# Performance work log

Measured on AMD Instinct MI355X. Metric: run time of the kernel, lower is better.

## Reference

```python
import jax, jax.numpy as jnp
import numpy as np

DEPTH_REF = jnp.array([28.01, 16.32], dtype=jnp.float32)
DIM_REF = jnp.array([[3.88, 1.63, 1.53], [0.84, 1.76, 0.66], [1.78, 1.52, 1.78]], dtype=jnp.float32)
TOPK = 50
DET_THRESHOLD = 0.25
PI = 3.14159265358979


def nms_hm(heat, kernel=3):
    # 3x3 max-pool NMS: keep peaks, zero everything else
    pad = (kernel - 1) // 2
    hmax = jax.lax.reduce_window(heat, -jnp.inf, jax.lax.max,
                                 (1, 1, kernel, kernel), (1, 1, 1, 1),
                                 [(0, 0), (0, 0), (pad, pad), (pad, pad)])
    return jnp.where(hmax == heat, heat, 0.0)


def select_topk(heat, K):
    B, C, H, W = heat.shape
    scores_all, inds_all = jax.lax.top_k(heat.reshape(B, C, H * W), K)  # [B,C,K]
    ys_all = (inds_all // W).astype(jnp.float32)
    xs_all = (inds_all % W).astype(jnp.float32)
    scores, inds = jax.lax.top_k(scores_all.reshape(B, C * K), K)       # [B,K] over classes
    clses = (inds // K).astype(jnp.float32)
    topk_inds = jnp.take_along_axis(inds_all.reshape(B, C * K), inds, axis=1)
    ys = jnp.take_along_axis(ys_all.reshape(B, C * K), inds, axis=1)
    xs = jnp.take_along_axis(xs_all.reshape(B, C * K), inds, axis=1)
    return scores, topk_inds, clses, ys, xs


def select_point_of_interest(index, feature_maps):
    B, Cf, H, W = feature_maps.shape
    fm = feature_maps.transpose(0, 2, 3, 1).reshape(B, H * W, Cf)
    return jnp.take_along_axis(fm, index[:, :, None], axis=1)  # [B,K,Cf]


def encode_box3d(rotys, dims, locs):
    # dims = (l, h, w); corner signs reproduce SMOKE's gather pattern
    N = rotys.shape[0]
    c, s = jnp.cos(rotys), jnp.sin(rotys)
    z, o = jnp.zeros_like(c), jnp.ones_like(c)
    ry = jnp.stack([c, z, s, z, o, z, -s, z, c], axis=1).reshape(N, 3, 3)
    sx = jnp.array([-0.5, 0.5, 0.5, 0.5, 0.5, -0.5, -0.5, -0.5], dtype=dims.dtype)
    sy = jnp.array([-1., -1., 0., 0., -1., -1., 0., 0.], dtype=dims.dtype)
    sz = jnp.array([-0.5, -0.5, -0.5, 0.5, 0.5, 0.5, 0.5, -0.5], dtype=dims.dtype)
    corners = jnp.stack([dims[:, 0:1] * sx, dims[:, 1:2] * sy, dims[:, 2:3] * sz], axis=1)  # [N,3,8]
    return jnp.einsum('nij,njk->nik', ry, corners) + locs[:, :, None]


def setup_inputs() -> dict:
    key = jax.random.key(0)
    k1, k2 = jax.random.split(key)
    B, C, H, W = 32, 3, 192, 640
    IMG_W, IMG_H = 4 * W, 4 * H
    pred_heatmap = jax.random.uniform(k1, (B, C, H, W), dtype=jnp.float32)
    pred_regression = jax.random.normal(k2, (B, 8, H, W), dtype=jnp.float32) * 0.5
    # affine image->heatmap (scale 1/4), invertible
    tm = jnp.array([[0.25, 0., 0.], [0., 0.25, 0.], [0., 0., 1.]], dtype=jnp.float32)
    trans_mat = jnp.tile(tm[None], (B, 1, 1))
    Kc = jnp.array([[721.5, 0., IMG_W / 2.], [0., 721.5, IMG_H / 2.], [0., 0., 1.]], dtype=jnp.float32)
    K_mat = jnp.tile(Kc[None], (B, 1, 1))
    img_size = jnp.tile(jnp.array([[IMG_W, IMG_H]], dtype=jnp.float32), (B, 1))
    return {"pred_heatmap": pred_heatmap, "pred_regression": pred_regression,
            "trans_mat": trans_mat, "K_mat": K_mat, "img_size": img_size}


def reference(pred_heatmap, pred_regression, trans_mat, K_mat, img_size):
    B = pred_heatmap.shape[0]
    heat = nms_hm(pred_heatmap)
    scores, inds, clses, ys, xs = select_topk(heat, TOPK)
    reg = select_point_of_interest(inds, pred_regression).reshape(-1, 8)  # [B*K,8]

    points = jnp.stack([xs.reshape(-1), ys.reshape(-1)], axis=1)          # heatmap coords
    depth_off, proj_off = reg[:, 0], reg[:, 1:3]
    dim_off, ori = reg[:, 3:6], reg[:, 6:8]
    cls_idx = clses.reshape(-1).astype(jnp.int32)

    obj_id = jnp.repeat(jnp.arange(B), TOPK)
    tm_inv = jnp.linalg.inv(trans_mat)[obj_id]   # [N,3,3]
    K_inv = jnp.linalg.inv(K_mat)[obj_id]

    # decode location: heatmap -> image -> camera frame
    proj = points + proj_off
    proj_ext = jnp.concatenate([proj, jnp.ones_like(proj[:, :1])], axis=1)
    proj_img = jnp.einsum('nij,nj->ni', tm_inv, proj_ext)                 # image-plane homog coords
    depths = depth_off * DEPTH_REF[1] + DEPTH_REF[0]
    locs = jnp.einsum('nij,nj->ni', K_inv, proj_img * depths[:, None])

    dims = jnp.exp(dim_off) * DIM_REF[cls_idx]                            # (l,h,w)
    locs = locs.at[:, 1].add(dims[:, 1] / 2)

    # decode orientation
    eps = 1e-7
    rays = jnp.arctan(locs[:, 0] / (locs[:, 2] + eps))
    alphas = jnp.arctan(ori[:, 0] / (ori[:, 1] + eps))
    alphas = jnp.where(ori[:, 1] >= 0, alphas - PI / 2, alphas + PI / 2)
    rotys = alphas + rays
    wrap = lambda a: jnp.where(a > PI, a - 2 * PI, jnp.where(a < -PI, a + 2 * PI, a))
    rotys, alphas = wrap(rotys), wrap(alphas)

    # encode 2D boxes from projected 3D corners
    corners = encode_box3d(rotys, dims, locs)                             # [N,3,8]
    proj2 = jnp.einsum('nij,njk->nik', K_mat[obj_id], corners)
    xy = proj2[:, :2] / proj2[:, 2:3]
    Wi, Hi = img_size[obj_id, 0], img_size[obj_id, 1]
    xmins = jnp.clip(xy[:, 0].min(axis=1), 0.0, Wi)
    ymins = jnp.clip(xy[:, 1].min(axis=1), 0.0, Hi)
    xmaxs = jnp.clip(xy[:, 0].max(axis=1), 0.0, Wi)
    ymaxs = jnp.clip(xy[:, 1].max(axis=1), 0.0, Hi)
    box2d = jnp.stack([xmins, ymins, xmaxs, ymaxs], axis=1)

    dims_rolled = jnp.roll(dims, -1, axis=1)                              # (h,w,l)
    result = jnp.concatenate([
        cls_idx.astype(jnp.float32)[:, None], alphas[:, None], box2d,
        dims_rolled, locs, rotys[:, None], scores.reshape(-1, 1)], axis=1)  # [B*K,14]
    keep = result[:, -1] > DET_THRESHOLD
    return jnp.where(keep[:, None], result, 0.0)
```

## Files before the change

kernel.cpp:

```cpp
#include <hip/hip_runtime.h>
#include <math.h>

#define Hd 192
#define Wd 640
#define HWp (Hd * Wd)
#define NCLS 3
#define KTOP 50
#define NB 32
#define NPL (NB * NCLS)
#define SPR 40
#define TSTR (Hd * SPR)
#define NSUB 6
#define SSTR (TSTR / NSUB)
#define CAPS 512
#define CAP 2048
#define RBK 256
#define GPR 160
#define GPP (HWp / 4)
#define NMERGE (NCLS * NSUB * KTOP)
#define TH_F 0.995f
#define PI_F 3.14159265358979f

#define OFF_SSC 0
#define OFF_SPI 0x40000
#define OFF_SCNT 0x80000

__device__ inline float fmax3(float a, float b, float c) {
  return fmaxf(fmaxf(a, b), c);
}

__device__ inline unsigned long long mk_key(unsigned int bits, int idx) {
  return ((unsigned long long)bits << 32) | (unsigned int)~idx;
}

__device__ inline int bucket_of(unsigned int bits) {
  const unsigned int base = __float_as_uint(TH_F);
  if (bits <= base) return 0;
  unsigned int d = (bits - base) >> 9;
  return d > 255u ? 255 : (int)d;
}

__device__ inline unsigned long long mk_key19(unsigned int bits, int cls, int idx) {
  return ((unsigned long long)bits << 19) |
         ((unsigned long long)(2 - cls) << 17) |
         (unsigned long long)((idx ^ 0x1FFFF) & 0x1FFFF);
}

struct Row16 {
  float4 q0, q1, q2, q3;
  float l, r;
};

__device__ inline Row16 load_row16(const float* __restrict__ rp, int x0, bool valid) {
  Row16 o;
  if (valid) {
    o.q0 = *(const float4*)(rp);
    o.q1 = *(const float4*)(rp + 4);
    o.q2 = *(const float4*)(rp + 8);
    o.q3 = *(const float4*)(rp + 12);
    o.l = (x0 > 0) ? rp[-1] : -INFINITY;
    o.r = (x0 + 16 < Wd) ? rp[16] : -INFINITY;
  } else {
    o.q0.x = o.q0.y = o.q0.z = o.q0.w = -INFINITY;
    o.q1 = o.q0; o.q2 = o.q0; o.q3 = o.q0;
    o.l = -INFINITY; o.r = -INFINITY;
  }
  return o;
}

__device__ inline float4 max3v(const float4 a, const float4 b, const float4 c) {
  float4 o;
  o.x = fmax3(a.x, b.x, c.x);
  o.y = fmax3(a.y, b.y, c.y);
  o.z = fmax3(a.z, b.z, c.z);
  o.w = fmax3(a.w, b.w, c.w);
  return o;
}

template <typename F>
__device__ inline void strip_peaks(const float* __restrict__ hp, int strip, F&& f) {
  const int y = strip / SPR;
  const int x0 = (strip - y * SPR) * 16;
  const float* pm = hp + y * Wd + x0;
  const Row16 m = load_row16(pm, x0, true);
  const Row16 t = load_row16(pm - Wd, x0, y > 0);
  const Row16 b = load_row16(pm + Wd, x0, y < Hd - 1);
  const float cl = fmax3(t.l, m.l, b.l);
  const float cr = fmax3(t.r, m.r, b.r);
  const float4 c0 = max3v(t.q0, m.q0, b.q0);
  const float4 c1 = max3v(t.q1, m.q1, b.q1);
  const float4 c2 = max3v(t.q2, m.q2, b.q2);
  const float4 c3 = max3v(t.q3, m.q3, b.q3);
  const int base = y * Wd + x0;
#define EMIT(V, W0, W1, W2, J)                                       \
  if ((V) >= TH_F && (V) == fmax3((W0), (W1), (W2)))                 \
    f(__float_as_uint(V), base + (J));
  EMIT(m.q0.x, cl,   c0.x, c0.y, 0)
  EMIT(m.q0.y, c0.x, c0.y, c0.z, 1)
  EMIT(m.q0.z, c0.y, c0.z, c0.w, 2)
  EMIT(m.q0.w, c0.z, c0.w, c1.x, 3)
  EMIT(m.q1.x, c0.w, c1.x, c1.y, 4)
  EMIT(m.q1.y, c1.x, c1.y, c1.z, 5)
  EMIT(m.q1.z, c1.y, c1.z, c1.w, 6)
  EMIT(m.q1.w, c1.z, c1.w, c2.x, 7)
  EMIT(m.q2.x, c1.w, c2.x, c2.y, 8)
  EMIT(m.q2.y, c2.x, c2.y, c2.z, 9)
  EMIT(m.q2.z, c2.y, c2.z, c2.w, 10)
  EMIT(m.q2.w, c2.z, c2.w, c3.x, 11)
  EMIT(m.q3.x, c2.w, c3.x, c3.y, 12)
  EMIT(m.q3.y, c3.x, c3.y, c3.z, 13)
  EMIT(m.q3.z, c3.y, c3.z, c3.w, 14)
  EMIT(m.q3.w, c3.z, c3.w, cr,   15)
#undef EMIT
}

template <typename F>
__device__ inline void peaks_in_group(const float* __restrict__ p, int g, F&& f) {
  const int y = g / GPR;
  const int x0 = (g - y * GPR) * 4;
  const float* rm = p + y * Wd + x0;
  const float4 mq = *(const float4*)rm;
  const float ml = (x0 > 0) ? rm[-1] : -INFINITY;
  const float mr = (x0 + 4 < Wd) ? rm[4] : -INFINITY;
  float4 tq; float tl, tr;
  if (y > 0) {
    const float* rt = rm - Wd;
    tq = *(const float4*)rt;
    tl = (x0 > 0) ? rt[-1] : -INFINITY;
    tr = (x0 + 4 < Wd) ? rt[4] : -INFINITY;
  } else {
    tq.x = tq.y = tq.z = tq.w = -INFINITY; tl = -INFINITY; tr = -INFINITY;
  }
  float4 bq; float bl, br;
  if (y < Hd - 1) {
    const float* rb = rm + Wd;
    bq = *(const float4*)rb;
    bl = (x0 > 0) ? rb[-1] : -INFINITY;
    br = (x0 + 4 < Wd) ? rb[4] : -INFINITY;
  } else {
    bq.x = bq.y = bq.z = bq.w = -INFINITY; bl = -INFINITY; br = -INFINITY;
  }
  const float c0 = fmax3(tl, ml, bl);
  const float c1 = fmax3(tq.x, mq.x, bq.x);
  const float c2 = fmax3(tq.y, mq.y, bq.y);
  const float c3 = fmax3(tq.z, mq.z, bq.z);
  const float c4 = fmax3(tq.w, mq.w, bq.w);
  const float c5 = fmax3(tr, mr, br);
  const int base = y * Wd + x0;
  if (mq.x == fmax3(c0, c1, c2)) f(__float_as_uint(mq.x), base + 0);
  if (mq.y == fmax3(c1, c2, c3)) f(__float_as_uint(mq.y), base + 1);
  if (mq.z == fmax3(c2, c3, c4)) f(__float_as_uint(mq.z), base + 2);
  if (mq.w == fmax3(c3, c4, c5)) f(__float_as_uint(mq.w), base + 3);
}

template <typename F>
__device__ inline void for_each_peak_plane(const float* __restrict__ p, int tid,
                                           int nth, F&& f) {
  for (int g = tid; g < GPP; g += nth) peaks_in_group(p, g, f);
}

__device__ inline void inv3(const float* m, float* o) {
  float a = m[0], b = m[1], c = m[2];
  float d = m[3], e = m[4], f = m[5];
  float g = m[6], h = m[7], i = m[8];
  float A = e * i - f * h;
  float B = -(d * i - f * g);
  float C = d * h - e * g;
  float det = a * A + b * B + c * C;
  float id = 1.0f / det;
  o[0] = A * id;            o[1] = -(b * i - c * h) * id; o[2] = (b * f - c * e) * id;
  o[3] = B * id;            o[4] = (a * i - c * g) * id;  o[5] = -(a * f - c * d) * id;
  o[6] = C * id;            o[7] = -(a * h - b * g) * id; o[8] = (a * e - b * d) * id;
}

__device__ inline float wrap_pi(float a) {
  if (a > PI_F) return a - 2.0f * PI_F;
  if (a < -PI_F) return a + 2.0f * PI_F;
  return a;
}

__constant__ float DIM_REF_C[9] = {3.88f, 1.63f, 1.53f,
                                   0.84f, 1.76f, 0.66f,
                                   1.78f, 1.52f, 1.78f};

__global__ __launch_bounds__(256) void scanrank_kernel(
    const float* __restrict__ heat,
    float* __restrict__ ssc,
    int* __restrict__ spi,
    int* __restrict__ scnt) {
  const int blk = blockIdx.x;
  const int tid = threadIdx.x;
  const int plane = blk / NSUB;
  const int sub = blk - plane * NSUB;
  const float* hp = heat + (size_t)plane * HWp;
  const int sbase = sub * SSTR;

  __shared__ unsigned long long s_key[CAPS];
  __shared__ unsigned long long c_key[CAPS];
  __shared__ int cnt[RBK], suf[RBK], cur[RBK];
  __shared__ int s_n, s_B, s_above, s_T;

  if (tid == 0) s_n = 0;
  __syncthreads();

  for (int it = 0; it < SSTR / 256; ++it) {
    const int strip = sbase + it * 256 + tid;
    strip_peaks(hp, strip, [&](unsigned int bits, int idx) {
      int slot = atomicAdd(&s_n, 1);
      if (slot < CAPS) s_key[slot] = mk_key(bits, idx);
    });
  }
  __syncthreads();
  int n = s_n;

  if (n > CAPS) {
    unsigned int* hist = (unsigned int*)c_key;
    const unsigned int THB = __float_as_uint(TH_F);
    for (int i = tid; i < 1024; i += 256) hist[i] = 0;
    __syncthreads();
    for (int it = 0; it < SSTR / 256; ++it) {
      const int strip = sbase + it * 256 + tid;
      strip_peaks(hp, strip, [&](unsigned int bits, int idx) {
        atomicAdd(&hist[(bits - THB) >> 7], 1u);
      });
    }
    __syncthreads();
    if (tid == 0) {
      int acc = 0, res = 0, above = 0;
      for (int q = 655; q >= 0; --q) {
        int cc = (int)hist[q];
        if (acc + cc >= KTOP) { res = q; above = acc; break; }
        acc += cc;
      }
      s_B = res; s_above = above;
    }
    __syncthreads();
    const int Bc = s_B;
    for (int i = tid; i < 1024; i += 256) hist[i] = 0;
    __syncthreads();
    for (int it = 0; it < SSTR / 256; ++it) {
      const int strip = sbase + it * 256 + tid;
      strip_peaks(hp, strip, [&](unsigned int bits, int idx) {
        if ((int)((bits - THB) >> 7) == Bc)
          atomicAdd(&hist[(bits - THB) & 127], 1u);
      });
    }
    __syncthreads();
    if (tid == 0) {
      int acc = s_above, S = 0;
      for (int sb = 127; sb >= 0; --sb) {
        int cc = (int)hist[sb];
        if (acc + cc >= KTOP) { S = sb; break; }
        acc += cc;
      }
      s_T = (int)(THB + ((unsigned int)Bc << 7) + (unsigned int)S);
      s_n = 0;
    }
    __syncthreads();
    const unsigned int T = (unsigned int)s_T;
    for (int it = 0; it < SSTR / 256; ++it) {
      const int strip = sbase + it * 256 + tid;
      strip_peaks(hp, strip, [&](unsigned int bits, int idx) {
        if (bits >= T) {
          int slot = atomicAdd(&s_n, 1);
          if (slot < CAPS) s_key[slot] = mk_key(bits, idx);
        }
      });
    }
    __syncthreads();
    n = s_n < CAPS ? s_n : CAPS;
  }

  cnt[tid] = 0;
  cur[tid] = 0;
  __syncthreads();
  for (int i = tid; i < n; i += 256)
    atomicAdd(&cnt[bucket_of((unsigned int)(s_key[i] >> 32))], 1);
  __syncthreads();
  suf[tid] = cnt[tid];
  __syncthreads();
#pragma unroll
  for (int d = 1; d < RBK; d <<= 1) {
    const int v = (tid + d < RBK) ? suf[tid + d] : 0;
    __syncthreads();
    suf[tid] += v;
    __syncthreads();
  }
  {
    const int excl = suf[tid] - cnt[tid];
    __syncthreads();
    suf[tid] = excl;
  }
  __syncthreads();
  for (int i = tid; i < n; i += 256) {
    const unsigned long long k = s_key[i];
    const int bq = bucket_of((unsigned int)(k >> 32));
    const int slot = suf[bq] + atomicAdd(&cur[bq], 1);
    c_key[slot] = k;
  }
  __syncthreads();
  float* psc = ssc + blk * 64;
  int* ppi = spi + blk * 64;
  for (int i = tid; i < n; i += 256) {
    const unsigned long long k = c_key[i];
    const int bq = bucket_of((unsigned int)(k >> 32));
    const int st = suf[bq];
    const int nb = cnt[bq];
    int rank = st;
    for (int tt = st; tt < st + nb; ++tt) rank += (c_key[tt] > k);
    if (rank < KTOP) {
      psc[rank] = __uint_as_float((unsigned int)(k >> 32));
      ppi[rank] = (int)~((unsigned int)k);
    }
  }
  for (int s2 = n + tid; s2 < KTOP; s2 += 256) {
    psc[s2] = 0.0f;
    ppi[s2] = 0;
  }
  if (tid == 0) scnt[blk] = n;
}

__global__ __launch_bounds__(256) void decode_kernel(
    const float* __restrict__ heat,
    const float* __restrict__ ssc,
    const int* __restrict__ spi,
    const int* __restrict__ scnt,
    const float* __restrict__ regr,
    const float* __restrict__ trans_mat,
    const float* __restrict__ K_mat,
    const float* __restrict__ img_size,
    float* __restrict__ out) {
  const int b = blockIdx.x;
  const int tid = threadIdx.x;

  __shared__ unsigned long long d_keys[NMERGE];
  __shared__ unsigned long long g_keys[NMERGE];
  __shared__ int cnt[RBK], suf[RBK], cur[RBK];
  __shared__ int sel[KTOP];
  __shared__ int s_ctl[NCLS * NSUB];
  __shared__ int s_ct[NCLS];
  __shared__ unsigned long long s_key[CAP];
  __shared__ unsigned long long c_key[CAP];
  __shared__ int s_fbB, s_fbAbove, s_fbT, s_fbCnt;

  if (tid < NCLS * NSUB) s_ctl[tid] = scnt[b * NCLS * NSUB + tid];
  __syncthreads();
  if (tid < NCLS) {
    int t = 0;
#pragma unroll
    for (int s = 0; s < NSUB; ++s) t += s_ctl[tid * NSUB + s];
    s_ct[tid] = t;
  }
  __syncthreads();

  for (int i = tid; i < NMERGE; i += 256) {
    const int c = i / (NSUB * KTOP);
    const int rem = i - c * (NSUB * KTOP);
    const int s = rem / KTOP;
    const int k2 = rem - s * KTOP;
    const int sb = (b * NCLS + c) * NSUB + s;
    const float v = ssc[sb * 64 + k2];
    const int idx = spi[sb * 64 + k2];
    d_keys[i] = mk_key19(__float_as_uint(v), c, idx);
  }
  __syncthreads();

  for (int c = 0; c < NCLS; ++c) {
    if (s_ct[c] < KTOP) {
      const float* hp = heat + (size_t)(b * NCLS + c) * HWp;
      unsigned int* fb_hist = (unsigned int*)c_key;
      for (int i = tid; i < 1024; i += 256) fb_hist[i] = 0;
      __syncthreads();
      for_each_peak_plane(hp, tid, 256, [&](unsigned int bits, int idx) {
        unsigned int bkt = bits >> 20; if (bkt > 1023u) bkt = 1023u;
        atomicAdd(&fb_hist[bkt], 1u);
      });
      __syncthreads();
      if (tid == 0) {
        int acc = 0, Bs = -1;
        for (int bkt = 1023; bkt >= 0; --bkt) {
          int cc = (int)fb_hist[bkt];
          if (acc + cc >= KTOP) { Bs = bkt; s_fbAbove = acc; break; }
          acc += cc;
        }
        s_fbB = Bs;
        if (Bs < 0) s_fbAbove = acc;
      }
      __syncthreads();
      const int Bs = s_fbB;
      unsigned int T;
      if (Bs < 0) {
        T = 0;
      } else {
        for (int i = tid; i < 1024; i += 256) fb_hist[i] = 0;
        __syncthreads();
        for_each_peak_plane(hp, tid, 256, [&](unsigned int bits, int idx) {
          unsigned int bkt = bits >> 20; if (bkt > 1023u) bkt = 1023u;
          if ((int)bkt == Bs) atomicAdd(&fb_hist[(bits >> 10) & 1023], 1u);
        });
        __syncthreads();
        if (tid == 0) {
          int acc = s_fbAbove, Ss = 0;
          for (int sb = 1023; sb >= 0; --sb) {
            int cc = (int)fb_hist[sb];
            if (acc + cc >= KTOP) { Ss = sb; break; }
            acc += cc;
          }
          s_fbT = (int)(((unsigned int)Bs << 20) | ((unsigned int)Ss << 10));
        }
        __syncthreads();
        T = (unsigned int)s_fbT;
      }
      if (tid == 0) s_fbCnt = 0;
      __syncthreads();
      for_each_peak_plane(hp, tid, 256, [&](unsigned int bits, int idx) {
        if (bits >= T) {
          int slot = atomicAdd(&s_fbCnt, 1);
          if (slot < CAP) s_key[slot] = mk_key(bits, idx);
        }
      });
      __syncthreads();
      const int M = s_fbCnt < CAP ? s_fbCnt : CAP;
      cnt[tid] = 0; cur[tid] = 0;
      __syncthreads();
      for (int i = tid; i < M; i += 256)
        atomicAdd(&cnt[bucket_of((unsigned int)(s_key[i] >> 32))], 1);
      __syncthreads();
      suf[tid] = cnt[tid];
      __syncthreads();
#pragma unroll
      for (int d = 1; d < RBK; d <<= 1) {
        const int v = (tid + d < RBK) ? suf[tid + d] : 0;
        __syncthreads();
        suf[tid] += v;
        __syncthreads();
      }
      {
        const int excl = suf[tid] - cnt[tid];
        __syncthreads();
        suf[tid] = excl;
      }
      __syncthreads();
      for (int i = tid; i < M; i += 256) {
        const unsigned long long k = s_key[i];
        const int bq = bucket_of((unsigned int)(k >> 32));
        const int slot = suf[bq] + atomicAdd(&cur[bq], 1);
        c_key[slot] = k;
      }
      __syncthreads();
      for (int i = tid; i < NSUB * KTOP; i += 256)
        d_keys[c * (NSUB * KTOP) + i] = mk_key19(0u, c, 0);
      __syncthreads();
      for (int i = tid; i < M; i += 256) {
        const unsigned long long k = c_key[i];
        const int bq = bucket_of((unsigned int)(k >> 32));
        const int st = suf[bq];
        const int nb = cnt[bq];
        int rank = st;
        for (int tt = st; tt < st + nb; ++tt) rank += (c_key[tt] > k);
        if (rank < KTOP)
          d_keys[c * (NSUB * KTOP) + rank] =
              mk_key19((unsigned int)(k >> 32), c, (int)~((unsigned int)k));
      }
      __syncthreads();
    }
  }

  cnt[tid] = 0;
  cur[tid] = 0;
  __syncthreads();
  for (int i = tid; i < NMERGE; i += 256)
    atomicAdd(&cnt[bucket_of((unsigned int)(d_keys[i] >> 19))], 1);
  __syncthreads();
  suf[tid] = cnt[tid];
  __syncthreads();
#pragma unroll
  for (int d = 1; d < RBK; d <<= 1) {
    const int v = (tid + d < RBK) ? suf[tid + d] : 0;
    __syncthreads();
    suf[tid] += v;
    __syncthreads();
  }
  {
    const int excl = suf[tid] - cnt[tid];
    __syncthreads();
    suf[tid] = excl;
  }
  __syncthreads();
  for (int i = tid; i < NMERGE; i += 256) {
    const unsigned long long k = d_keys[i];
    const int bq = bucket_of((unsigned int)(k >> 19));
    const int slot = suf[bq] + atomicAdd(&cur[bq], 1);
    g_keys[slot] = k;
  }
  __syncthreads();
  for (int i = tid; i < NMERGE; i += 256) {
    const unsigned long long k = g_keys[i];
    const int bq = bucket_of((unsigned int)(k >> 19));
    const int st = suf[bq];
    if (st >= KTOP) continue;
    const int nb = cnt[bq];
    int rank = st;
    for (int tt = st; tt < st + nb; ++tt) rank += (g_keys[tt] > k);
    if (rank < KTOP) sel[rank] = i;
  }
  __syncthreads();

  if (tid < KTOP) {
    const unsigned long long k = g_keys[sel[tid]];
    const float score = __uint_as_float((unsigned int)(k >> 19));
    const int cls = 2 - (int)((k >> 17) & 3);
    const int ind = ((int)(k & 0x1FFFF)) ^ 0x1FFFF;
    const float ys = (float)(ind / Wd);
    const float xs = (float)(ind - (ind / Wd) * Wd);

    const float* rb = regr + (size_t)b * 8 * HWp + ind;
    const float r0 = rb[0 * HWp], r1 = rb[1 * HWp], r2 = rb[2 * HWp], r3 = rb[3 * HWp];
    const float r4 = rb[4 * HWp], r5 = rb[5 * HWp], r6 = rb[6 * HWp], r7 = rb[7 * HWp];

    float tm[9], km[9], tmi[9], kmi[9];
#pragma unroll
    for (int q = 0; q < 9; ++q) { tm[q] = trans_mat[b * 9 + q]; km[q] = K_mat[b * 9 + q]; }
    inv3(tm, tmi);
    inv3(km, kmi);

    const float px = xs + r1, py = ys + r2;
    const float gx = tmi[0] * px + tmi[1] * py + tmi[2];
    const float gy = tmi[3] * px + tmi[4] * py + tmi[5];
    const float gz = tmi[6] * px + tmi[7] * py + tmi[8];
    const float depth = r0 * 16.32f + 28.01f;
    const float qx = gx * depth, qy = gy * depth, qz = gz * depth;
    const float lx = kmi[0] * qx + kmi[1] * qy + kmi[2] * qz;
    float ly = kmi[3] * qx + kmi[4] * qy + kmi[5] * qz;
    const float lz = kmi[6] * qx + kmi[7] * qy + kmi[8] * qz;

    const float d0 = expf(r3) * DIM_REF_C[cls * 3 + 0];
    const float d1 = expf(r4) * DIM_REF_C[cls * 3 + 1];
    const float d2 = expf(r5) * DIM_REF_C[cls * 3 + 2];
    ly += d1 * 0.5f;

    const float ray = atanf(lx / (lz + 1e-7f));
    float alpha = atanf(r6 / (r7 + 1e-7f));
    alpha += (r7 >= 0.0f) ? -PI_F * 0.5f : PI_F * 0.5f;
    const float roty = wrap_pi(alpha + ray);
    alpha = wrap_pi(alpha);

    const float SX[8] = {-0.5f, 0.5f, 0.5f, 0.5f, 0.5f, -0.5f, -0.5f, -0.5f};
    const float SY[8] = {-1.0f, -1.0f, 0.0f, 0.0f, -1.0f, -1.0f, 0.0f, 0.0f};
    const float SZ[8] = {-0.5f, -0.5f, -0.5f, 0.5f, 0.5f, 0.5f, 0.5f, -0.5f};
    const float cr = cosf(roty), sr = sinf(roty);
    float minx = INFINITY, maxx = -INFINITY, miny = INFINITY, maxy = -INFINITY;
#pragma unroll
    for (int j = 0; j < 8; ++j) {
      const float ax = d0 * SX[j], ay = d1 * SY[j], az = d2 * SZ[j];
      const float cx = cr * ax + sr * az + lx;
      const float cy = ay + ly;
      const float cz = -sr * ax + cr * az + lz;
      const float ppx = km[0] * cx + km[1] * cy + km[2] * cz;
      const float ppy = km[3] * cx + km[4] * cy + km[5] * cz;
      const float ppz = km[6] * cx + km[7] * cy + km[8] * cz;
      const float X = ppx / ppz, Y = ppy / ppz;
      minx = fminf(minx, X); maxx = fmaxf(maxx, X);
      miny = fminf(miny, Y); maxy = fmaxf(maxy, Y);
    }
    const float Wi = img_size[b * 2 + 0], Hi = img_size[b * 2 + 1];
    const float xmin = fminf(fmaxf(minx, 0.0f), Wi);
    const float ymin = fminf(fmaxf(miny, 0.0f), Hi);
    const float xmax = fminf(fmaxf(maxx, 0.0f), Wi);
    const float ymax = fminf(fmaxf(maxy, 0.0f), Hi);

    float* o = out + (size_t)(b * KTOP + tid) * 14;
    if (score > 0.25f) {
      o[0] = (float)cls; o[1] = alpha;
      o[2] = xmin; o[3] = ymin; o[4] = xmax; o[5] = ymax;
      o[6] = d1; o[7] = d2; o[8] = d0;
      o[9] = lx; o[10] = ly; o[11] = lz;
      o[12] = roty; o[13] = score;
    } else {
#pragma unroll
      for (int q = 0; q < 14; ++q) o[q] = 0.0f;
    }
  }
}


extern "C" void kernel_launch(void* const* d_in, const int* in_sizes, int n_in,
                              void* d_out, int out_size, void* d_ws, size_t ws_size,
                              hipStream_t stream) {
  const float* heat = (const float*)d_in[0];
  const float* regr = (const float*)d_in[1];
  const float* tmat = (const float*)d_in[2];
  const float* kmat = (const float*)d_in[3];
  const float* isz = (const float*)d_in[4];

  char* ws = (char*)d_ws;
  float* ssc = (float*)(ws + OFF_SSC);
  int* spi = (int*)(ws + OFF_SPI);
  int* scnt = (int*)(ws + OFF_SCNT);

  scanrank_kernel<<<NPL * NSUB, 256, 0, stream>>>(heat, ssc, spi, scnt);
  decode_kernel<<<NB, 256, 0, stream>>>(heat, ssc, spi, scnt,
                                        regr, tmat, kmat, isz,
                                        (float*)d_out);
}
```

Baseline: 211.4 us.

## Scan heatmap in row bands with sliding row window for peak detection

Replaces independent 16-wide strip NMS evaluation with a per-thread vertical sliding window over 4 rows, reusing the top and middle rows in registers across iterations. Each block now covers a 24-row band, and the plane is split into 8 blocks instead of 6. This is meant to cut redundant global loads of neighbouring rows. In exchange, 16 threads per block idle and the longer per-thread serial chain may reduce memory-level parallelism.

```diff
diff --git a/kernel.cpp b/kernel.cpp
--- a/kernel.cpp
+++ b/kernel.cpp
@@ -8,10 +8,10 @@
 #define KTOP 50
 #define NB 32
 #define NPL (NB * NCLS)
-#define SPR 40
-#define TSTR (Hd * SPR)
-#define NSUB 6
-#define SSTR (TSTR / NSUB)
+#define NSUB 8
+#define BROWS 24
+#define NCOL 40
+#define NACT (NCOL * 6)
 #define CAPS 512
 #define CAP 2048
 #define RBK 256
@@ -78,40 +78,52 @@
 }
 
 template <typename F>
-__device__ inline void strip_peaks(const float* __restrict__ hp, int strip, F&& f) {
-  const int y = strip / SPR;
-  const int x0 = (strip - y * SPR) * 16;
-  const float* pm = hp + y * Wd + x0;
-  const Row16 m = load_row16(pm, x0, true);
-  const Row16 t = load_row16(pm - Wd, x0, y > 0);
-  const Row16 b = load_row16(pm + Wd, x0, y < Hd - 1);
-  const float cl = fmax3(t.l, m.l, b.l);
-  const float cr = fmax3(t.r, m.r, b.r);
-  const float4 c0 = max3v(t.q0, m.q0, b.q0);
-  const float4 c1 = max3v(t.q1, m.q1, b.q1);
-  const float4 c2 = max3v(t.q2, m.q2, b.q2);
-  const float4 c3 = max3v(t.q3, m.q3, b.q3);
-  const int base = y * Wd + x0;
+__device__ inline void band_scan(const float* __restrict__ hp, int band,
+                                 int tid, F&& f) {
+  if (tid >= NACT) return;
+  const int c = tid % NCOL;
+  const int rg = tid / NCOL;
+  const int r0 = band * BROWS + rg * 4;
+  const int x0 = c * 16;
+  const float* colp = hp + x0;
+
+  Row16 rt = load_row16(colp + (long)(r0 - 1) * Wd, x0, r0 > 0);
+  Row16 rm = load_row16(colp + (long)r0 * Wd, x0, true);
+#pragma unroll
+  for (int j = 0; j < 4; ++j) {
+    const int y = r0 + j;
+    const Row16 rb = load_row16(colp + (long)(y + 1) * Wd, x0, y + 1 < Hd);
+
+    const float cl = fmax3(rt.l, rm.l, rb.l);
+    const float cr = fmax3(rt.r, rm.r, rb.r);
+    const float4 c0 = max3v(rt.q0, rm.q0, rb.q0);
+    const float4 c1 = max3v(rt.q1, rm.q1, rb.q1);
+    const float4 c2 = max3v(rt.q2, rm.q2, rb.q2);
+    const float4 c3 = max3v(rt.q3, rm.q3, rb.q3);
+    const int base = y * Wd + x0;
 #define EMIT(V, W0, W1, W2, J)                                       \
-  if ((V) >= TH_F && (V) == fmax3((W0), (W1), (W2)))                 \
-    f(__float_as_uint(V), base + (J));
-  EMIT(m.q0.x, cl,   c0.x, c0.y, 0)
-  EMIT(m.q0.y, c0.x, c0.y, c0.z, 1)
-  EMIT(m.q0.z, c0.y, c0.z, c0.w, 2)
-  EMIT(m.q0.w, c0.z, c0.w, c1.x, 3)
-  EMIT(m.q1.x, c0.w, c1.x, c1.y, 4)
-  EMIT(m.q1.y, c1.x, c1.y, c1.z, 5)
-  EMIT(m.q1.z, c1.y, c1.z, c1.w, 6)
-  EMIT(m.q1.w, c1.z, c1.w, c2.x, 7)
-  EMIT(m.q2.x, c1.w, c2.x, c2.y, 8)
-  EMIT(m.q2.y, c2.x, c2.y, c2.z, 9)
-  EMIT(m.q2.z, c2.y, c2.z, c2.w, 10)
-  EMIT(m.q2.w, c2.z, c2.w, c3.x, 11)
-  EMIT(m.q3.x, c2.w, c3.x, c3.y, 12)
-  EMIT(m.q3.y, c3.x, c3.y, c3.z, 13)
-  EMIT(m.q3.z, c3.y, c3.z, c3.w, 14)
-  EMIT(m.q3.w, c3.z, c3.w, cr,   15)
+    if ((V) >= TH_F && (V) == fmax3((W0), (W1), (W2)))               \
+      f(__float_as_uint(V), base + (J));
+    EMIT(rm.q0.x, cl,   c0.x, c0.y, 0)
+    EMIT(rm.q0.y, c0.x, c0.y, c0.z, 1)
+    EMIT(rm.q0.z, c0.y, c0.z, c0.w, 2)
+    EMIT(rm.q0.w, c0.z, c0.w, c1.x, 3)
+    EMIT(rm.q1.x, c0.w, c1.x, c1.y, 4)
+    EMIT(rm.q1.y, c1.x, c1.y, c1.z, 5)
+    EMIT(rm.q1.z, c1.y, c1.z, c1.w, 6)
+    EMIT(rm.q1.w, c1.z, c1.w, c2.x, 7)
+    EMIT(rm.q2.x, c1.w, c2.x, c2.y, 8)
+    EMIT(rm.q2.y, c2.x, c2.y, c2.z, 9)
+    EMIT(rm.q2.z, c2.y, c2.z, c2.w, 10)
+    EMIT(rm.q2.w, c2.z, c2.w, c3.x, 11)
+    EMIT(rm.q3.x, c2.w, c3.x, c3.y, 12)
+    EMIT(rm.q3.y, c3.x, c3.y, c3.z, 13)
+    EMIT(rm.q3.z, c3.y, c3.z, c3.w, 14)
+    EMIT(rm.q3.w, c3.z, c3.w, cr,   15)
 #undef EMIT
+    rt = rm;
+    rm = rb;
+  }
 }
 
 template <typename F>
@@ -191,9 +203,8 @@
   const int blk = blockIdx.x;
   const int tid = threadIdx.x;
   const int plane = blk / NSUB;
-  const int sub = blk - plane * NSUB;
+  const int band = blk - plane * NSUB;
   const float* hp = heat + (size_t)plane * HWp;
-  const int sbase = sub * SSTR;
 
   __shared__ unsigned long long s_key[CAPS];
   __shared__ unsigned long long c_key[CAPS];
@@ -203,13 +214,10 @@
   if (tid == 0) s_n = 0;
   __syncthreads();
 
-  for (int it = 0; it < SSTR / 256; ++it) {
-    const int strip = sbase + it * 256 + tid;
-    strip_peaks(hp, strip, [&](unsigned int bits, int idx) {
-      int slot = atomicAdd(&s_n, 1);
-      if (slot < CAPS) s_key[slot] = mk_key(bits, idx);
-    });
-  }
+  band_scan(hp, band, tid, [&](unsigned int bits, int idx) {
+    int slot = atomicAdd(&s_n, 1);
+    if (slot < CAPS) s_key[slot] = mk_key(bits, idx);
+  });
   __syncthreads();
   int n = s_n;
 
@@ -218,12 +226,9 @@
     const unsigned int THB = __float_as_uint(TH_F);
     for (int i = tid; i < 1024; i += 256) hist[i] = 0;
     __syncthreads();
-    for (int it = 0; it < SSTR / 256; ++it) {
-      const int strip = sbase + it * 256 + tid;
-      strip_peaks(hp, strip, [&](unsigned int bits, int idx) {
-        atomicAdd(&hist[(bits - THB) >> 7], 1u);
-      });
-    }
+    band_scan(hp, band, tid, [&](unsigned int bits, int idx) {
+      atomicAdd(&hist[(bits - THB) >> 7], 1u);
+    });
     __syncthreads();
     if (tid == 0) {
       int acc = 0, res = 0, above = 0;
@@ -238,13 +243,10 @@
     const int Bc = s_B;
     for (int i = tid; i < 1024; i += 256) hist[i] = 0;
     __syncthreads();
-    for (int it = 0; it < SSTR / 256; ++it) {
-      const int strip = sbase + it * 256 + tid;
-      strip_peaks(hp, strip, [&](unsigned int bits, int idx) {
-        if ((int)((bits - THB) >> 7) == Bc)
-          atomicAdd(&hist[(bits - THB) & 127], 1u);
-      });
-    }
+    band_scan(hp, band, tid, [&](unsigned int bits, int idx) {
+      if ((int)((bits - THB) >> 7) == Bc)
+        atomicAdd(&hist[(bits - THB) & 127], 1u);
+    });
     __syncthreads();
     if (tid == 0) {
       int acc = s_above, S = 0;
@@ -258,15 +260,12 @@
     }
     __syncthreads();
     const unsigned int T = (unsigned int)s_T;
-    for (int it = 0; it < SSTR / 256; ++it) {
-      const int strip = sbase + it * 256 + tid;
-      strip_peaks(hp, strip, [&](unsigned int bits, int idx) {
-        if (bits >= T) {
-          int slot = atomicAdd(&s_n, 1);
-          if (slot < CAPS) s_key[slot] = mk_key(bits, idx);
-        }
-      });
-    }
+    band_scan(hp, band, tid, [&](unsigned int bits, int idx) {
+      if (bits >= T) {
+        int slot = atomicAdd(&s_n, 1);
+        if (slot < CAPS) s_key[slot] = mk_key(bits, idx);
+      }
+    });
     __syncthreads();
     n = s_n < CAPS ? s_n : CAPS;
   }
```

Result: faster. 200.7 us (-5.0%).
